# Performance work log

Measured on AMD Instinct MI355X. Metric: run time of the kernel, lower is better.

## Reference

```python
import jax, jax.numpy as jnp
import numpy as np
from jax import lax

EPS = 2e-05


def _conv2d(x, w, b, stride):
    # x: [B,C,H,W], w: [O,I,3,3] (OIHW), VALID padding
    y = lax.conv_general_dilated(x, w, (stride, stride), 'VALID',
                                 dimension_numbers=('NCHW', 'OIHW', 'NCHW'))
    return y + b[None, :, None, None]


def _reflect_pad(x):
    return jnp.pad(x, ((0, 0), (0, 0), (1, 1), (1, 1)), mode='reflect')


def _transfer(cont_feat, styl_feat):
    # cont_feat, styl_feat: [B, N, H, W]
    B, N, H, W = cont_feat.shape
    xc = cont_feat.reshape(B, N, -1)   # [B,N,Mc]
    xs = styl_feat.reshape(B, N, -1)   # [B,N,Ms]
    I = jnp.eye(N, dtype=xc.dtype)

    # whitening of content
    mc = jnp.mean(xc, axis=-1, keepdims=True)
    xc0 = xc - mc
    cov_c = jnp.einsum('bnm,bkm->bnk', xc0, xc0) / (xc0.shape[-1] - 1)
    Lc = jnp.linalg.cholesky(cov_c + EPS * I)  # eps*I regularization (torch retry loop)
    inv_Lc = jnp.linalg.inv(Lc)
    whiten = jnp.einsum('bnk,bkm->bnm', inv_Lc, xc0)

    # coloring with style statistics
    ms = jnp.mean(xs, axis=-1, keepdims=True)
    xs0 = xs - ms
    cov_s = jnp.einsum('bnm,bkm->bnk', xs0, xs0) / (xs0.shape[-1] - 1)
    Ls = jnp.linalg.cholesky(cov_s + EPS * I)
    colored = jnp.einsum('bnk,bkm->bnm', Ls, whiten) + ms
    return colored.reshape(B, N, H, W)


def setup_inputs() -> dict:
    key = jax.random.key(0)
    k1, k2, k3, k4 = jax.random.split(key, 4)
    B, C, H, W = 8, 128, 256, 256
    cont_feat = jax.random.normal(k1, (B, C, H, W), dtype=jnp.float32)
    styl_feat = jax.random.normal(k2, (B, C, H, W), dtype=jnp.float32)
    # conv params (kaiming-ish scaling)
    fan1 = C * 9
    W1 = jax.random.normal(k3, (C, C, 3, 3), dtype=jnp.float32) / np.sqrt(fan1)
    b1 = jnp.zeros((C,), dtype=jnp.float32)
    W2 = jax.random.normal(k4, (2 * C, C, 3, 3), dtype=jnp.float32) / np.sqrt(fan1)
    b2 = jnp.zeros((2 * C,), dtype=jnp.float32)
    return {'cont_feat': cont_feat, 'styl_feat': styl_feat,
            'W1': W1, 'b1': b1, 'W2': W2, 'b2': b2}


def reference(cont_feat, styl_feat, W1, b1, W2, b2):
    cs = _transfer(cont_feat, styl_feat)          # [B,C,H,W]
    x = _conv2d(_reflect_pad(cs), W1, b1, 2)      # [B,C,H/2,W/2]
    x = jax.nn.relu(x)
    out = _conv2d(_reflect_pad(x), W2, b2, 1)     # [B,2C,H/2,W/2]
    return out
```

## Files before the change

### kernel.cpp

```cpp
#include <hip/hip_runtime.h>
#include <hip/hip_bf16.h>

#define B_  8
#define C_  128
#define M_  65536
#define EPSV 2e-05f

typedef __attribute__((ext_vector_type(8))) short bf16x8;
typedef __attribute__((ext_vector_type(4))) float f32x4;

#define MFMA(a, b, c) __builtin_amdgcn_mfma_f32_16x16x32_bf16((a), (b), (c), 0, 0, 0)

__device__ __forceinline__ short f2b(float f) {
    unsigned u = __float_as_uint(f);
    u = (u + 0x7FFFu + ((u >> 16) & 1u)) >> 16;
    return (short)u;
}

__device__ __forceinline__ int swz(int px, int c) {
    return px * 256 + ((((c >> 3) ^ (px & 15)) << 4) | ((c & 7) << 1));
}

__device__ __forceinline__ int rot(int i, int k) {
    return i * 128 + ((((k >> 2) + i) & 31) << 2) + (k & 3);
}

__global__ __launch_bounds__(256) void k_prep(const float* W1, const float* W2,
                                              short* wp1, short* wp2) {
    int idx = blockIdx.x * 256 + threadIdx.x;
    if (idx < 9 * 128 * 128) {
        int c = idx & 127, o = (idx >> 7) & 127, rs = idx >> 14;
        wp1[idx] = f2b(W1[(o * 128 + c) * 9 + rs]);
    }
    idx -= 9 * 128 * 128;
    if (idx >= 0 && idx < 9 * 256 * 128) {
        int c = idx & 127, o = (idx >> 7) & 255, rs = idx >> 15;
        wp2[idx] = f2b(W2[(o * 128 + c) * 9 + rs]);
    }
}

__global__ __launch_bounds__(256, 2) void k_gram(const float* Xsrc, int which,
                                                 float* part, float* S) {
    __shared__ short ls[128 * 264];
    int bx = blockIdx.x;
    int chunk = bx & 31, b = bx >> 5;
    const float* X = Xsrc + (size_t)b * C_ * M_ + chunk * 2048;
    int tid = threadIdx.x, lane = tid & 63, wid = tid >> 6;

    float sacc[32];
    #pragma unroll
    for (int p = 0; p < 32; ++p) sacc[p] = 0.f;
    f32x4 acc[2][8];
    for (int u = 0; u < 2; ++u)
        for (int j = 0; j < 8; ++j) acc[u][j] = (f32x4){0.f, 0.f, 0.f, 0.f};

    float4 pfA[8], pfB[8];

#define GLOAD(pf, g)                                                              \
    _Pragma("unroll")                                                             \
    for (int p = 0; p < 8; ++p)                                                   \
        pf[p] = *(const float4*)(X + (size_t)(wid + 4 * ((g) * 8 + p)) * M_ +     \
                                 kb + lane * 4);

#define GSTORE(pf, g)                                                             \
    _Pragma("unroll")                                                             \
    for (int p = 0; p < 8; ++p) {                                                 \
        int row = wid + 4 * ((g) * 8 + p);                                        \
        float4 v = pf[p];                                                         \
        sacc[(g) * 8 + p] += v.x + v.y + v.z + v.w;                               \
        union { __hip_bfloat162 h[2]; unsigned long long u; } pk;                 \
        pk.h[0] = __float22bfloat162_rn(make_float2(v.x, v.y));                   \
        pk.h[1] = __float22bfloat162_rn(make_float2(v.z, v.w));                   \
        *(unsigned long long*)(ls + row * 264 + lane * 4) = pk.u;                 \
    }

    for (int it = 0; it < 8; ++it) {
        int kb = it * 256;
        GLOAD(pfA, 0)
        GLOAD(pfB, 1)
        GSTORE(pfA, 0)
        GLOAD(pfA, 2)
        GSTORE(pfB, 1)
        GLOAD(pfB, 3)
        GSTORE(pfA, 2)
        GSTORE(pfB, 3)
        asm volatile("s_waitcnt lgkmcnt(0)" ::: "memory");
        __builtin_amdgcn_sched_barrier(0);
        __builtin_amdgcn_s_barrier();
        for (int ks = 0; ks < 8; ++ks) {
            int co = ks * 32 + (lane >> 4) * 8;
            bf16x8 a[2], bbf[8];
            for (int u = 0; u < 2; ++u) {
                int row = (wid * 2 + u) * 16 + (lane & 15);
                a[u] = *(const bf16x8*)(ls + row * 264 + co);
            }
            for (int j = 0; j < 8; ++j) {
                int row = j * 16 + (lane & 15);
                bbf[j] = *(const bf16x8*)(ls + row * 264 + co);
            }
            for (int u = 0; u < 2; ++u)
                for (int j = 0; j < 8; ++j)
                    acc[u][j] = MFMA(a[u], bbf[j], acc[u][j]);
        }
        __builtin_amdgcn_sched_barrier(0);
        __builtin_amdgcn_s_barrier();
    }
#undef GLOAD
#undef GSTORE
    float* Sp = S + ((size_t)which * 8 + b) * 128;
    #pragma unroll
    for (int p = 0; p < 32; ++p) {
        float s = sacc[p];
        s += __shfl_xor(s, 1); s += __shfl_xor(s, 2);
        s += __shfl_xor(s, 4); s += __shfl_xor(s, 8);
        s += __shfl_xor(s, 16); s += __shfl_xor(s, 32);
        if (lane == 0) atomicAdd(&Sp[wid + 4 * p], s);
    }
    float* Pp = part + ((size_t)((which * 8 + b) * 32 + chunk)) * 16384;
    for (int u = 0; u < 2; ++u) {
        int rowb = (wid * 2 + u) * 16 + (lane >> 4) * 4;
        for (int j = 0; j < 8; ++j) {
            int col = j * 16 + (lane & 15);
            for (int e = 0; e < 4; ++e)
                Pp[(rowb + e) * 128 + col] = acc[u][j][e];
        }
    }
}

__global__ __launch_bounds__(256) void k_gsum(const float* part, float* G) {
    int idx = blockIdx.x * 256 + threadIdx.x;
    int m = idx >> 14, e = idx & 16383;
    const float* p = part + (size_t)m * 32 * 16384 + e;
    float s = 0.f;
    #pragma unroll
    for (int c = 0; c < 32; ++c) s += p[(size_t)c * 16384];
    G[idx] = s;
}

__global__ __launch_bounds__(256) void k_solve(const float* G, const float* S,
                                               short* Tb, float* Vv) {
    __shared__ float A[16384];
    __shared__ float Bm[16384];
    __shared__ float muA[128], muB[128];
    int b = blockIdx.x;
    int tid = threadIdx.x;
    int half = tid >> 7, i = tid & 127;
    const float invM = 1.f / 65536.f;
    const float invM1 = 1.f / 65535.f;
    float* M = half ? Bm : A;
    float* mu = half ? muB : muA;
    const float* Gp = G + ((size_t)(half * 8 + b)) * 16384;
    const float* Sp = S + ((size_t)(half * 8 + b)) * 128;

    mu[i] = Sp[i] * invM;
    __syncthreads();

    {
        const float4* G4 = (const float4*)Gp;
        int c4 = i & 31;
        #pragma unroll 4
        for (int bt = 0; bt < 4; ++bt) {
            float4 gv[8];
            #pragma unroll
            for (int q = 0; q < 8; ++q) gv[q] = G4[i + 128 * (bt * 8 + q)];
            #pragma unroll
            for (int q = 0; q < 8; ++q) {
                int it = bt * 8 + q;
                int r = (i >> 5) + 4 * it;
                float mur = mu[r] * 65536.f;
                float4 mc = *(const float4*)&mu[c4 * 4];
                float4 g = gv[q], cv;
                cv.x = (g.x - mur * mc.x) * invM1;
                cv.y = (g.y - mur * mc.y) * invM1;
                cv.z = (g.z - mur * mc.z) * invM1;
                cv.w = (g.w - mur * mc.w) * invM1;
                int c0 = c4 * 4;
                if (r == c0 + 0) cv.x += EPSV;
                if (r == c0 + 1) cv.y += EPSV;
                if (r == c0 + 2) cv.z += EPSV;
                if (r == c0 + 3) cv.w += EPSV;
                *(float4*)(M + r * 128 + (((c4 + r) & 31) << 2)) = cv;
            }
        }
    }
    __syncthreads();

    #pragma unroll 1
    for (int bb = 0; bb < 4; ++bb) {
        const int jb0 = bb * 32, bend = jb0 + 32;
        float t[32], u[32], t0[32];
        #pragma unroll
        for (int g = 0; g < 8; ++g) {
            float4 v = *(const float4*)(M + i * 128 + ((((jb0 >> 2) + g + i) & 31) << 2));
            t0[g * 4 + 0] = v.x; t0[g * 4 + 1] = v.y;
            t0[g * 4 + 2] = v.z; t0[g * 4 + 3] = v.w;
        }
        #pragma unroll
        for (int jj = 0; jj < 32; ++jj) {
            const int j = jb0 + jj;
            float dot = 0.f;
            #pragma unroll
            for (int kk = 0; kk < jj; ++kk)
                dot += u[kk] * M[rot(j, jb0 + kk)];
            float raw = t0[jj] - dot;
            if (i >= j) M[rot(i, j)] = raw;
            __syncthreads();
            float pr = M[rot(j, j)];
            float piv = sqrtf(pr);
            float rpj = 1.f / piv;
            float tv = (i > j) ? raw * rpj : (i == j ? piv : 0.f);
            t[jj] = tv;
            u[jj] = tv * rpj;
        }
        #pragma unroll
        for (int g = 0; g < 8; ++g) {
            float4 v = {t[g * 4], t[g * 4 + 1], t[g * 4 + 2], t[g * 4 + 3]};
            *(float4*)(M + i * 128 + ((((jb0 >> 2) + g + i) & 31) << 2)) =
                (i >= jb0) ? v : *(float4*)(M + i * 128 + ((((jb0 >> 2) + g + i) & 31) << 2));
        }
        __syncthreads();
        if (bb < 3) {
            if (i >= bend) {
                int jmax = (i & ~63) + 64;
                for (int j4 = bend; j4 < jmax; j4 += 4) {
                    float* rp_ = M + i * 128 + ((((j4 >> 2) + i) & 31) << 2);
                    float4 r = *(float4*)rp_;
                    #pragma unroll
                    for (int g = 0; g < 8; ++g) {
                        int kc = (jb0 >> 2) + g;
                        float4 c0 = *(const float4*)(M + (j4 + 0) * 128 + (((kc + j4 + 0) & 31) << 2));
                        float4 c1 = *(const float4*)(M + (j4 + 1) * 128 + (((kc + j4 + 1) & 31) << 2));
                        float4 c2 = *(const float4*)(M + (j4 + 2) * 128 + (((kc + j4 + 2) & 31) << 2));
                        float4 c3 = *(const float4*)(M + (j4 + 3) * 128 + (((kc + j4 + 3) & 31) << 2));
                        float ta = t[g * 4], tb = t[g * 4 + 1], tc = t[g * 4 + 2], td = t[g * 4 + 3];
                        r.x -= ta * c0.x + tb * c0.y + tc * c0.z + td * c0.w;
                        r.y -= ta * c1.x + tb * c1.y + tc * c1.z + td * c1.w;
                        r.z -= ta * c2.x + tb * c2.y + tc * c2.z + td * c2.w;
                        r.w -= ta * c3.x + tb * c3.y + tc * c3.z + td * c3.w;
                    }
                    *(float4*)rp_ = r;
                }
            }
            __syncthreads();
        }
    }
    __syncthreads();

    float rdia = 0.f, tii = 0.f;
    if (half == 0) {
        rdia = 1.f / A[rot(i, i)];
        tii = Bm[rot(i, i)] * rdia;
    }
    __syncthreads();
    if (half == 0) {
        A[rot(i, i)] = rdia;
        Bm[rot(i, i)] = tii;
    }
    __syncthreads();

    #pragma unroll 1
    for (int b2 = 3; b2 >= 0; --b2) {
        const int jb0 = b2 * 32, bend = jb0 + 32;
        if (half == 0) {
            float t[32], l0[32];
            #pragma unroll
            for (int g = 0; g < 8; ++g) {
                float4 v = *(const float4*)(Bm + i * 128 + ((((jb0 >> 2) + g + i) & 31) << 2));
                l0[g * 4 + 0] = v.x; l0[g * 4 + 1] = v.y;
                l0[g * 4 + 2] = v.z; l0[g * 4 + 3] = v.w;
            }
            #pragma unroll
            for (int jj = 31; jj >= 0; --jj) {
                const int j = jb0 + jj;
                float dot = (i < bend) ? tii * A[rot(i, j)] : 0.f;
                #pragma unroll
                for (int kk = jj + 1; kk < 32; ++kk) {
                    const int k = jb0 + kk;
                    dot += t[kk] * A[rot(k, j)];
                }
                float val = (l0[jj] - dot) * A[rot(j, j)];
                t[jj] = (j < i) ? val : (j == i ? tii : 0.f);
            }
            #pragma unroll
            for (int g = 0; g < 8; ++g) {
                float4 v = {t[g * 4], t[g * 4 + 1], t[g * 4 + 2], t[g * 4 + 3]};
                *(float4*)(Bm + i * 128 + ((((jb0 >> 2) + g + i) & 31) << 2)) = v;
            }
        }
        __syncthreads();
        if (jb0 > 0) {
            if (i >= jb0) {
                float th[32];
                #pragma unroll
                for (int g = 0; g < 8; ++g) {
                    float4 v = *(const float4*)(Bm + i * 128 + ((((jb0 >> 2) + g + i) & 31) << 2));
                    th[g * 4 + 0] = v.x; th[g * 4 + 1] = v.y;
                    th[g * 4 + 2] = v.z; th[g * 4 + 3] = v.w;
                }
                for (int j4 = half * 4; j4 < jb0; j4 += 8) {
                    float* rp = Bm + i * 128 + ((((j4 >> 2) + i) & 31) << 2);
                    float4 r = *(float4*)rp;
                    #pragma unroll
                    for (int kk = 0; kk < 32; ++kk) {
                        const int k = jb0 + kk;
                        float4 lc = *(const float4*)(A + k * 128 + ((((j4 >> 2) + k) & 31) << 2));
                        r.x -= th[kk] * lc.x; r.y -= th[kk] * lc.y;
                        r.z -= th[kk] * lc.z; r.w -= th[kk] * lc.w;
                    }
                    *(float4*)rp = r;
                }
            }
            __syncthreads();
        }
    }

    if (half == 0) {
        float vdot = 0.f;
        short* Tr = Tb + (size_t)b * 16384 + i * 128;
        for (int j4 = 0; j4 < 32; ++j4) {
            float4 tv = *(const float4*)(Bm + i * 128 + (((j4 + i) & 31) << 2));
            float4 mc = *(const float4*)&muA[j4 * 4];
            vdot += tv.x * mc.x + tv.y * mc.y + tv.z * mc.z + tv.w * mc.w;
            union { __hip_bfloat162 h[2]; unsigned long long u; } pk;
            pk.h[0] = __float22bfloat162_rn(make_float2(tv.x, tv.y));
            pk.h[1] = __float22bfloat162_rn(make_float2(tv.z, tv.w));
            *(unsigned long long*)(Tr + j4 * 4) = pk.u;
        }
        Vv[b * 128 + i] = muB[i] - vdot;
    }
}

__global__ __launch_bounds__(256) void k_transform(const float* cont, const short* Tb,
                                                   const float* Vv, short* colored) {
    __shared__ short ls[16384];
    char* lsb = (char*)ls;
    int bx = blockIdx.x;
    int b = bx >> 9, p0 = (bx & 511) << 7;
    int tid = threadIdx.x, lane = tid & 63, wid = tid >> 6;

    {
        int px = tid & 127, ch = tid >> 7;
        const float* Xp = cont + (size_t)b * C_ * M_ + p0 + px;
        for (int it = 0; it < 16; ++it) {
            int c0 = it * 8 + ch * 4;
            float x0 = Xp[(size_t)(c0 + 0) * M_];
            float x1 = Xp[(size_t)(c0 + 1) * M_];
            float x2 = Xp[(size_t)(c0 + 2) * M_];
            float x3 = Xp[(size_t)(c0 + 3) * M_];
            union { short s[4]; unsigned long long u; } pk;
            pk.s[0] = f2b(x0); pk.s[1] = f2b(x1); pk.s[2] = f2b(x2); pk.s[3] = f2b(x3);
            *(unsigned long long*)(lsb + swz(px, c0)) = pk.u;
        }
    }
    __syncthreads();
    f32x4 acc[8][2];
    for (int pg = 0; pg < 8; ++pg)
        for (int u = 0; u < 2; ++u) acc[pg][u] = (f32x4){0.f, 0.f, 0.f, 0.f};
    const short* Tbase = Tb + (size_t)b * 16384;
    for (int kc = 0; kc < 4; ++kc) {
        int co = kc * 32 + (lane >> 4) * 8;
        bf16x8 bfr[2], afr[8];
        for (int u = 0; u < 2; ++u) {
            int chn = (wid * 2 + u) * 16 + (lane & 15);
            bfr[u] = *(const bf16x8*)(Tbase + chn * 128 + co);
        }
        for (int pg = 0; pg < 8; ++pg) {
            int px = pg * 16 + (lane & 15);
            afr[pg] = *(const bf16x8*)(lsb + swz(px, co));
        }
        for (int pg = 0; pg < 8; ++pg)
            for (int u = 0; u < 2; ++u)
                acc[pg][u] = MFMA(afr[pg], bfr[u], acc[pg][u]);
    }
    __syncthreads();
    for (int u = 0; u < 2; ++u) {
        int chn = (wid * 2 + u) * 16 + (lane & 15);
        float vv = Vv[b * 128 + chn];
        for (int pg = 0; pg < 8; ++pg)
            for (int e = 0; e < 4; ++e) {
                int px = pg * 16 + (lane >> 4) * 4 + e;
                *(short*)(lsb + swz(px, chn)) = f2b(acc[pg][u][e] + vv);
            }
    }
    __syncthreads();
    short* dst = colored + ((size_t)b * M_ + p0) * 128;
    for (int it = 0; it < 8; ++it) {
        int gid = tid + it * 256;
        int px = gid >> 4, gr = gid & 15;
        bf16x8 v = *(const bf16x8*)(lsb + px * 256 + ((gr ^ (px & 15)) << 4));
        *(bf16x8*)(dst + (size_t)px * 128 + gr * 8) = v;
    }
}

__global__ __launch_bounds__(256) void k_conv1(const short* colored, const short* wp1,
                                               const float* b1, short* out1) {
    __shared__ short ls[130 * 128];
    char* lsb = (char*)ls;
    int x0 = blockIdx.x * 64, y = blockIdx.y, b = blockIdx.z;
    int tid = threadIdx.x, lane = tid & 63, wid = tid >> 6;

    f32x4 acc[4][2];
    for (int pg = 0; pg < 4; ++pg)
        for (int u = 0; u < 2; ++u) acc[pg][u] = (f32x4){0.f, 0.f, 0.f, 0.f};

    for (int r = 0; r < 3; ++r) {
        int grow = 2 * y - 1 + r;
        if (grow < 0) grow = -grow;
        __syncthreads();
        const short* src = colored + ((size_t)b * M_ + grow * 256) * 128;
        for (int it = 0; it < 9; ++it) {
            int gid = tid + it * 256;
            if (gid < 130 * 16) {
                int L = gid >> 4, gr = gid & 15;
                int gcol = 2 * x0 - 1 + L;
                if (gcol < 0) gcol = -gcol;
                else if (gcol > 255) gcol = 510 - gcol;
                bf16x8 v = *(const bf16x8*)(src + (size_t)gcol * 128 + gr * 8);
                *(bf16x8*)(lsb + L * 256 + ((gr ^ (L & 15)) << 4)) = v;
            }
        }
        __syncthreads();
        for (int s = 0; s < 3; ++s)
            for (int kc = 0; kc < 4; ++kc) {
                int co = kc * 32 + (lane >> 4) * 8;
                bf16x8 afr[4], bfr[2];
                for (int pg = 0; pg < 4; ++pg) {
                    int L = (pg * 16 + (lane & 15)) * 2 + s;
                    afr[pg] = *(const bf16x8*)(lsb + swz(L, co));
                }
                const short* wb = wp1 + (r * 3 + s) * 128 * 128;
                for (int u = 0; u < 2; ++u) {
                    int o = (wid * 2 + u) * 16 + (lane & 15);
                    bfr[u] = *(const bf16x8*)(wb + o * 128 + co);
                }
                for (int pg = 0; pg < 4; ++pg)
                    for (int u = 0; u < 2; ++u)
                        acc[pg][u] = MFMA(afr[pg], bfr[u], acc[pg][u]);
            }
    }
    __syncthreads();
    for (int u = 0; u < 2; ++u) {
        int o = (wid * 2 + u) * 16 + (lane & 15);
        float bias = b1[o];
        for (int pg = 0; pg < 4; ++pg)
            for (int e = 0; e < 4; ++e) {
                int px = pg * 16 + (lane >> 4) * 4 + e;
                float v = acc[pg][u][e] + bias;
                v = v > 0.f ? v : 0.f;
                *(short*)(lsb + swz(px, o)) = f2b(v);
            }
    }
    __syncthreads();
    short* dst = out1 + ((size_t)b * 16384 + y * 128 + x0) * 128;
    for (int it = 0; it < 4; ++it) {
        int gid = tid + it * 256;
        int px = gid >> 4, gr = gid & 15;
        bf16x8 v = *(const bf16x8*)(lsb + px * 256 + ((gr ^ (px & 15)) << 4));
        *(bf16x8*)(dst + (size_t)px * 128 + gr * 8) = v;
    }
}

__global__ __launch_bounds__(256) void k_conv2(const short* out1, const short* wp2,
                                               const float* b2, float* outp) {
    __shared__ short ls[130 * 128];
    char* lsb = (char*)ls;
    int y = blockIdx.x, b = blockIdx.y;
    int tid = threadIdx.x, lane = tid & 63, wid = tid >> 6;

    f32x4 acc[8][4];
    for (int pg = 0; pg < 8; ++pg)
        for (int u = 0; u < 4; ++u) acc[pg][u] = (f32x4){0.f, 0.f, 0.f, 0.f};

    for (int r = 0; r < 3; ++r) {
        int grow = y - 1 + r;
        if (grow < 0) grow = -grow;
        else if (grow > 127) grow = 254 - grow;
        __syncthreads();
        const short* src = out1 + ((size_t)b * 16384 + grow * 128) * 128;
        for (int it = 0; it < 9; ++it) {
            int gid = tid + it * 256;
            if (gid < 130 * 16) {
                int L = gid >> 4, gr = gid & 15;
                int gcol = L - 1;
                if (gcol < 0) gcol = -gcol;
                else if (gcol > 127) gcol = 254 - gcol;
                bf16x8 v = *(const bf16x8*)(src + (size_t)gcol * 128 + gr * 8);
                *(bf16x8*)(lsb + L * 256 + ((gr ^ (L & 15)) << 4)) = v;
            }
        }
        __syncthreads();
        for (int s = 0; s < 3; ++s)
            for (int kc = 0; kc < 4; ++kc) {
                int co = kc * 32 + (lane >> 4) * 8;
                bf16x8 afr[8], bfr[4];
                for (int pg = 0; pg < 8; ++pg) {
                    int L = pg * 16 + (lane & 15) + s;
                    afr[pg] = *(const bf16x8*)(lsb + swz(L, co));
                }
                const short* wb = wp2 + (r * 3 + s) * 256 * 128;
                for (int u = 0; u < 4; ++u) {
                    int o = (wid * 4 + u) * 16 + (lane & 15);
                    bfr[u] = *(const bf16x8*)(wb + o * 128 + co);
                }
                for (int pg = 0; pg < 8; ++pg)
                    for (int u = 0; u < 4; ++u)
                        acc[pg][u] = MFMA(afr[pg], bfr[u], acc[pg][u]);
            }
    }
    for (int u = 0; u < 4; ++u) {
        int o = (wid * 4 + u) * 16 + (lane & 15);
        float bias = b2[o];
        float* dst = outp + ((size_t)b * 256 + o) * 16384 + y * 128;
        for (int pg = 0; pg < 8; ++pg) {
            float4 v;
            v.x = acc[pg][u][0] + bias;
            v.y = acc[pg][u][1] + bias;
            v.z = acc[pg][u][2] + bias;
            v.w = acc[pg][u][3] + bias;
            *(float4*)(dst + pg * 16 + (lane >> 4) * 4) = v;
        }
    }
}

extern "C" void kernel_launch(void* const* d_in, const int* in_sizes, int n_in,
                              void* d_out, int out_size, void* d_ws, size_t ws_size,
                              hipStream_t stream) {
    const float* cont = (const float*)d_in[0];
    const float* styl = (const float*)d_in[1];
    const float* W1 = (const float*)d_in[2];
    const float* b1 = (const float*)d_in[3];
    const float* W2 = (const float*)d_in[4];
    const float* b2 = (const float*)d_in[5];
    float* outp = (float*)d_out;
    char* ws = (char*)d_ws;

    float* G       = (float*)(ws + 0x0);
    float* S       = (float*)(ws + 0x100000);
    short* Tb      = (short*)(ws + 0x110000);
    float* Vv      = (float*)(ws + 0x150000);
    short* wp1     = (short*)(ws + 0x160000);
    short* wp2     = (short*)(ws + 0x1A8000);
    short* colored = (short*)(ws + 0x400000);
    float* part    = (float*)(ws + 0x400000);
    short* out1    = (short*)(ws + 0x8400000);

    hipMemsetAsync(S, 0, 0x2000, stream);
    k_prep<<<1728, 256, 0, stream>>>(W1, W2, wp1, wp2);
    k_gram<<<256, 256, 0, stream>>>(styl, 1, part, S);
    k_gram<<<256, 256, 0, stream>>>(cont, 0, part, S);
    k_gsum<<<1024, 256, 0, stream>>>(part, G);
    k_solve<<<8, 256, 0, stream>>>(G, S, Tb, Vv);
    k_transform<<<4096, 256, 0, stream>>>(cont, Tb, Vv, colored);
    k_conv1<<<dim3(2, 128, 8), 256, 0, stream>>>(colored, wp1, b1, out1);
    k_conv2<<<dim3(128, 8), 256, 0, stream>>>(out1, wp2, b2, outp);
}
```

Measured before the change: 638.9 us.

## Emit transposed bf16 content from gram kernel and reuse it in transform

The content gram pass now also writes a pixel-major bf16 copy of the content tile it already has in LDS. The transform kernel reads this compact, contiguous copy instead of re-reading strided fp32 content, and overwrites it in place with the colored output. This removes a second full fp32 read of the large content tensor. In exchange, the gram kernel does extra LDS reads and global stores inside its main loop, and the partial-gram buffer moves to the out1 region to avoid aliasing.

```diff
diff --git a/kernel.cpp b/kernel.cpp
--- a/kernel.cpp
+++ b/kernel.cpp
@@ -40,7 +40,7 @@
 }
 
 __global__ __launch_bounds__(256, 2) void k_gram(const float* Xsrc, int which,
-                                                 float* part, float* S) {
+                                                 float* part, float* S, short* xt) {
     __shared__ short ls[128 * 264];
     int bx = blockIdx.x;
     int chunk = bx & 31, b = bx >> 5;
@@ -101,6 +101,24 @@
             for (int u = 0; u < 2; ++u)
                 for (int j = 0; j < 8; ++j)
                     acc[u][j] = MFMA(a[u], bbf[j], acc[u][j]);
+        }
+        if (xt) {
+            int h = tid >> 7, p = tid & 127;
+            int px0 = 2 * p;
+            short* xrow = xt + ((size_t)b * M_ + chunk * 2048 + it * 256 + px0) * 128 + h * 64;
+            #pragma unroll
+            for (int g8 = 0; g8 < 8; ++g8) {
+                bf16x8 lo, hi;
+                #pragma unroll
+                for (int e = 0; e < 8; ++e) {
+                    int c = h * 64 + g8 * 8 + e;
+                    unsigned w = *(const unsigned*)(ls + c * 264 + px0);
+                    lo[e] = (short)(w & 0xFFFF);
+                    hi[e] = (short)(w >> 16);
+                }
+                *(bf16x8*)(xrow + g8 * 8) = lo;
+                *(bf16x8*)(xrow + 128 + g8 * 8) = hi;
+            }
         }
         __builtin_amdgcn_sched_barrier(0);
         __builtin_amdgcn_s_barrier();
@@ -330,8 +348,8 @@
     }
 }
 
-__global__ __launch_bounds__(256) void k_transform(const float* cont, const short* Tb,
-                                                   const float* Vv, short* colored) {
+__global__ __launch_bounds__(256) void k_transform(short* xt, const short* Tb,
+                                                   const float* Vv) {
     __shared__ short ls[16384];
     char* lsb = (char*)ls;
     int bx = blockIdx.x;
@@ -339,17 +357,12 @@
     int tid = threadIdx.x, lane = tid & 63, wid = tid >> 6;
 
     {
-        int px = tid & 127, ch = tid >> 7;
-        const float* Xp = cont + (size_t)b * C_ * M_ + p0 + px;
-        for (int it = 0; it < 16; ++it) {
-            int c0 = it * 8 + ch * 4;
-            float x0 = Xp[(size_t)(c0 + 0) * M_];
-            float x1 = Xp[(size_t)(c0 + 1) * M_];
-            float x2 = Xp[(size_t)(c0 + 2) * M_];
-            float x3 = Xp[(size_t)(c0 + 3) * M_];
-            union { short s[4]; unsigned long long u; } pk;
-            pk.s[0] = f2b(x0); pk.s[1] = f2b(x1); pk.s[2] = f2b(x2); pk.s[3] = f2b(x3);
-            *(unsigned long long*)(lsb + swz(px, c0)) = pk.u;
+        int prow = tid >> 1, hh = (tid & 1) * 64;
+        const short* src = xt + ((size_t)b * M_ + p0 + prow) * 128 + hh;
+        #pragma unroll
+        for (int g8 = 0; g8 < 8; ++g8) {
+            bf16x8 v = *(const bf16x8*)(src + g8 * 8);
+            *(bf16x8*)(lsb + swz(prow, hh + g8 * 8)) = v;
         }
     }
     __syncthreads();
@@ -383,7 +396,7 @@
             }
     }
     __syncthreads();
-    short* dst = colored + ((size_t)b * M_ + p0) * 128;
+    short* dst = xt + ((size_t)b * M_ + p0) * 128;
     for (int it = 0; it < 8; ++it) {
         int gid = tid + it * 256;
         int px = gid >> 4, gr = gid & 15;
@@ -541,16 +554,16 @@
     short* wp1     = (short*)(ws + 0x160000);
     short* wp2     = (short*)(ws + 0x1A8000);
     short* colored = (short*)(ws + 0x400000);
-    float* part    = (float*)(ws + 0x400000);
     short* out1    = (short*)(ws + 0x8400000);
+    float* part    = (float*)(ws + 0x8400000);
 
     hipMemsetAsync(S, 0, 0x2000, stream);
     k_prep<<<1728, 256, 0, stream>>>(W1, W2, wp1, wp2);
-    k_gram<<<256, 256, 0, stream>>>(styl, 1, part, S);
-    k_gram<<<256, 256, 0, stream>>>(cont, 0, part, S);
+    k_gram<<<256, 256, 0, stream>>>(styl, 1, part, S, nullptr);
+    k_gram<<<256, 256, 0, stream>>>(cont, 0, part, S, colored);
     k_gsum<<<1024, 256, 0, stream>>>(part, G);
     k_solve<<<8, 256, 0, stream>>>(G, S, Tb, Vv);
-    k_transform<<<4096, 256, 0, stream>>>(cont, Tb, Vv, colored);
+    k_transform<<<4096, 256, 0, stream>>>(colored, Tb, Vv);
     k_conv1<<<dim3(2, 128, 8), 256, 0, stream>>>(colored, wp1, b1, out1);
     k_conv2<<<dim3(128, 8), 256, 0, stream>>>(out1, wp2, b2, outp);
 }
```

New measurement: 675.2 us. 5.7% more time.
